# Performance work log

Measured on AMD Instinct MI355X. Metric: run time of the kernel, lower is better.

## Reference

```python
import jax, jax.numpy as jnp
import numpy as np

EPS = 1e-8

def quaternion_normalize(q):
    # q: [..., 4] -> unit quaternion
    return q / (jnp.linalg.norm(q, axis=-1, keepdims=True) + EPS)

def quaternion_mul(q1, q2):
    # Hamilton product; q1, q2 broadcastable [..., 4]
    w1, x1, y1, z1 = q1[..., 0], q1[..., 1], q1[..., 2], q1[..., 3]
    w2, x2, y2, z2 = q2[..., 0], q2[..., 1], q2[..., 2], q2[..., 3]
    w = w1 * w2 - x1 * x2 - y1 * y2 - z1 * z2
    x = w1 * x2 + x1 * w2 + y1 * z2 - z1 * y2
    y = w1 * y2 - x1 * z2 + y1 * w2 + z1 * x2
    z = w1 * z2 + x1 * y2 - y1 * x2 + z1 * w2
    return jnp.stack([w, x, y, z], axis=-1)

def setup_inputs() -> dict:
    key = jax.random.key(0)
    ks = jax.random.split(key, 7)
    B, N, M, D = 2, 512, 512, 256
    return {
        "vision_feat": jax.random.normal(ks[0], (B, N, D), dtype=jnp.float32),
        "text_feat": jax.random.normal(ks[1], (B, M, D), dtype=jnp.float32),
        "Wv": jax.random.normal(ks[2], (D, D), dtype=jnp.float32) * (1.0 / np.sqrt(D)),
        "bv": jax.random.normal(ks[3], (D,), dtype=jnp.float32) * 0.01,
        "Wt": jax.random.normal(ks[4], (D, D), dtype=jnp.float32) * (1.0 / np.sqrt(D)),
        "bt": jax.random.normal(ks[5], (D,), dtype=jnp.float32) * 0.01,
        "h": jnp.float32(1.0),
    }

def reference(vision_feat, text_feat, Wv, bv, Wt, bt, h):
    B, N, D = vision_feat.shape
    M = text_feat.shape[1]
    heads = D // 4
    # project to spinors and normalize per-quaternion
    v_spinor = quaternion_normalize((vision_feat @ Wv.T + bv).reshape(B, N, heads, 4))
    t_spinor = quaternion_normalize((text_feat @ Wt.T + bt).reshape(B, M, heads, 4))
    # broadcast pairwise quaternion product v * conj(t): [B, N, M, heads, 4]
    v_exp = v_spinor[:, :, None]                      # [B, N, 1, heads, 4]
    t_conj = t_spinor[:, None, :] * jnp.array([1.0, -1.0, -1.0, -1.0], dtype=t_spinor.dtype)
    inner = quaternion_mul(v_exp, t_conj)             # [B, N, M, heads, 4]
    vec_norm = jnp.linalg.norm(inner[..., 1:], axis=-1)
    w = inner[..., 0]
    gamma = 2.0 * jnp.arctan2(vec_norm, w + EPS)
    interference = jnp.cos(gamma / 2.0) ** 2          # [B, N, M, heads]
    attn = jax.nn.softmax(interference.mean(axis=-1) / jnp.sqrt(jnp.float32(D)), axis=-1)  # [B, N, M]
    new_vision = jnp.matmul(attn, text_feat)                      # [B, N, D]
    new_text = jnp.matmul(attn.transpose(0, 2, 1), vision_feat)   # [B, M, D]
    out_vision = vision_feat + h * new_vision
    out_text = text_feat + h * new_text
    return (out_vision, out_text)
```

## Files before the change

### kernel.cpp

```cpp
#include <hip/hip_runtime.h>
#include <math.h>

#define EPS 1e-8f

typedef short bf16x8 __attribute__((ext_vector_type(8)));
typedef short bf16x4 __attribute__((ext_vector_type(4)));
typedef float f32x4  __attribute__((ext_vector_type(4)));

__device__ __forceinline__ short f2bf(float f) {
    union { float fv; unsigned u; } v; v.fv = f;
    unsigned r = v.u + 0x7fffu + ((v.u >> 16) & 1u);
    return (short)(r >> 16);
}
__device__ __forceinline__ float bf2f(short s) {
    union { unsigned u; float f; } v;
    v.u = ((unsigned)(unsigned short)s) << 16;
    return v.f;
}
__device__ __forceinline__ bf16x8 pack8(float4 a, float4 b) {
    bf16x8 p;
    p[0] = f2bf(a.x); p[1] = f2bf(a.y); p[2] = f2bf(a.z); p[3] = f2bf(a.w);
    p[4] = f2bf(b.x); p[5] = f2bf(b.y); p[6] = f2bf(b.z); p[7] = f2bf(b.w);
    return p;
}

__global__ __launch_bounds__(256) void proj_expand_kernel(
    const float* __restrict__ vis, const float* __restrict__ txt,
    const float* __restrict__ Wv, const float* __restrict__ bv,
    const float* __restrict__ Wt, const float* __restrict__ bt,
    short* __restrict__ expq)
{
    const int t = threadIdx.x, lane = t & 63, wave = t >> 6;
    const int w  = blockIdx.x * 4 + wave;
    const int rt = w >> 3;
    const int ct = w & 7;
    const int which = rt >> 6;
    const int r0 = (rt & 63) * 16;
    const int c0 = ct * 32;
    const float* X    = which ? txt : vis;
    const float* W    = which ? Wt : Wv;
    const float* bias = which ? bt : bv;
    short* Eo = expq + which * 1024 * 1024;

    const int mrow = lane & 15, quad = lane >> 4;

    const float* Arow  = X + (r0 + mrow) * 256 + 8 * quad;
    const float* Brow0 = W + (c0 + mrow) * 256 + 8 * quad;
    const float* Brow1 = W + (c0 + 16 + mrow) * 256 + 8 * quad;

    f32x4 acc[2] = {};
    #pragma unroll 4
    for (int k0 = 0; k0 < 256; k0 += 32) {
        float4 a0 = *(const float4*)(Arow + k0);
        float4 a1 = *(const float4*)(Arow + k0 + 4);
        float4 p0 = *(const float4*)(Brow0 + k0);
        float4 p1 = *(const float4*)(Brow0 + k0 + 4);
        float4 q0 = *(const float4*)(Brow1 + k0);
        float4 q1 = *(const float4*)(Brow1 + k0 + 4);
        bf16x8 af = pack8(a0, a1);
        bf16x8 b0 = pack8(p0, p1);
        bf16x8 b1 = pack8(q0, q1);
        acc[0] = __builtin_amdgcn_mfma_f32_16x16x32_bf16(af, b0, acc[0], 0, 0, 0);
        acc[1] = __builtin_amdgcn_mfma_f32_16x16x32_bf16(af, b1, acc[1], 0, 0, 0);
    }

    const int qbase = lane & ~3;
    #pragma unroll
    for (int j = 0; j < 2; ++j) {
        const int col  = c0 + 16 * j + mrow;
        const float bb = bias[col];
        const int head = col >> 2;
        #pragma unroll
        for (int reg = 0; reg < 4; ++reg) {
            const int row = r0 + quad * 4 + reg;
            float v = acc[j][reg] + bb;
            float s = v * v;
            s += __shfl_xor(s, 1, 64);
            s += __shfl_xor(s, 2, 64);
            float q = v * (1.f / (sqrtf(s) + EPS));
            float q0 = __shfl(q, qbase + 0, 64);
            float q1 = __shfl(q, qbase + 1, 64);
            float q2 = __shfl(q, qbase + 2, 64);
            float q3 = __shfl(q, qbase + 3, 64);
            bf16x4 p;
            p[0] = f2bf(q * q0); p[1] = f2bf(q * q1);
            p[2] = f2bf(q * q2); p[3] = f2bf(q * q3);
            *(bf16x4*)(Eo + row * 1024 + head * 16 + (col & 3) * 4) = p;
        }
    }
}

__global__ __launch_bounds__(256) void logits_kernel(
    const short* __restrict__ expq, short* __restrict__ E,
    short* __restrict__ ET, float* __restrict__ rs)
{
    const int t = threadIdx.x, lane = t & 63, wave = t >> 6;
    const int w  = blockIdx.x * 4 + wave;
    const int b  = w >> 9;
    const int nt = (w >> 4) & 31;
    const int mt = w & 15;
    const int r0 = nt * 16, c0 = mt * 32;
    const int mrow = lane & 15, quad = lane >> 4;

    const short* Ar  = expq + (b * 512 + r0 + mrow) * 1024 + 8 * quad;
    const short* Br0 = expq + (1024 + b * 512 + c0 + mrow) * 1024 + 8 * quad;
    const short* Br1 = Br0 + 16 * 1024;

    f32x4 acc[2] = {};
    #pragma unroll 4
    for (int k0 = 0; k0 < 1024; k0 += 32) {
        bf16x8 a  = *(const bf16x8*)(Ar  + k0);
        bf16x8 b0 = *(const bf16x8*)(Br0 + k0);
        bf16x8 b1 = *(const bf16x8*)(Br1 + k0);
        acc[0] = __builtin_amdgcn_mfma_f32_16x16x32_bf16(a, b0, acc[0], 0, 0, 0);
        acc[1] = __builtin_amdgcn_mfma_f32_16x16x32_bf16(a, b1, acc[1], 0, 0, 0);
    }

    float e[2][4];
    #pragma unroll
    for (int j = 0; j < 2; ++j)
        #pragma unroll
        for (int reg = 0; reg < 4; ++reg)
            e[j][reg] = __expf(acc[j][reg] * (1.f / 1024.f));

    #pragma unroll
    for (int j = 0; j < 2; ++j) {
        const int col = c0 + 16 * j + mrow;
        bf16x4 pe;
        #pragma unroll
        for (int reg = 0; reg < 4; ++reg) {
            pe[reg] = f2bf(e[j][reg]);
            const int row = r0 + quad * 4 + reg;
            E[(b * 512 + row) * 512 + col] = pe[reg];
        }
        *(bf16x4*)(ET + (b * 512 + col) * 512 + r0 + quad * 4) = pe;
    }
    #pragma unroll
    for (int reg = 0; reg < 4; ++reg) {
        float p = e[0][reg] + e[1][reg];
        p += __shfl_xor(p, 1, 64);
        p += __shfl_xor(p, 2, 64);
        p += __shfl_xor(p, 4, 64);
        p += __shfl_xor(p, 8, 64);
        if (mrow == 0) {
            const int row = r0 + quad * 4 + reg;
            rs[(b * 512 + row) * 16 + (c0 >> 5)] = p;
        }
    }
}

__global__ __launch_bounds__(256) void transpose_scale_kernel(
    const float* __restrict__ vis, const float* __restrict__ txt,
    const float* __restrict__ rs,
    short* __restrict__ txtT, short* __restrict__ visST,
    float* __restrict__ rinv)
{
    const int bx = blockIdx.x;
    const int mat = bx >> 6;
    const int b   = (bx >> 5) & 1;
    const int m0  = (bx & 31) * 16;
    const int t   = threadIdx.x;

    __shared__ float rsc[16];
    if (mat == 1) {
        if (t < 16) {
            const float* p = rs + (b * 512 + m0 + t) * 16;
            float s = 0.f;
            #pragma unroll
            for (int i = 0; i < 16; ++i) s += p[i];
            const float ri = 1.f / s;
            rsc[t] = ri;
            rinv[b * 512 + m0 + t] = ri;
        }
        __syncthreads();
    }

    const float* src = (mat ? vis : txt) + (b * 512 + m0) * 256 + t;
    short* dst = (mat ? visST : txtT) + (b * 256 + t) * 512 + m0;

    bf16x8 v0, v1;
    #pragma unroll
    for (int i = 0; i < 8; ++i) {
        float a = src[i * 256];
        float c = src[(i + 8) * 256];
        if (mat) { a *= rsc[i]; c *= rsc[i + 8]; }
        v0[i] = f2bf(a);
        v1[i] = f2bf(c);
    }
    *(bf16x8*)(dst)     = v0;
    *(bf16x8*)(dst + 8) = v1;
}

__global__ __launch_bounds__(256) void out_kernel(
    const float* __restrict__ vis, const float* __restrict__ txt,
    const short* __restrict__ E, const short* __restrict__ ET,
    const short* __restrict__ txtT, const short* __restrict__ visST,
    const float* __restrict__ rinv, const float* __restrict__ hptr,
    float* __restrict__ outv, float* __restrict__ outt)
{
    const int t = threadIdx.x, lane = t & 63, wave = t >> 6;
    const int w     = blockIdx.x * 4 + wave;
    const int which = w >> 9;
    const int b     = (w >> 8) & 1;
    const int nt    = (w >> 3) & 31;
    const int dt    = w & 7;
    const int r0 = nt * 16, c0 = dt * 32;
    const int mrow = lane & 15, quad = lane >> 4;
    const float hv = hptr[0];

    const short* Ar  = (which ? ET : E) + (b * 512 + r0 + mrow) * 512 + 8 * quad;
    const short* Br0 = (which ? visST : txtT) + (b * 256 + c0 + mrow) * 512 + 8 * quad;
    const short* Br1 = Br0 + 16 * 512;
    const float* base = (which ? txt : vis) + (b * 512 + r0) * 256;
    float*       out  = (which ? outt : outv) + (b * 512 + r0) * 256;

    f32x4 acc[2] = {};
    #pragma unroll 4
    for (int k0 = 0; k0 < 512; k0 += 32) {
        bf16x8 a  = *(const bf16x8*)(Ar  + k0);
        bf16x8 b0 = *(const bf16x8*)(Br0 + k0);
        bf16x8 b1 = *(const bf16x8*)(Br1 + k0);
        acc[0] = __builtin_amdgcn_mfma_f32_16x16x32_bf16(a, b0, acc[0], 0, 0, 0);
        acc[1] = __builtin_amdgcn_mfma_f32_16x16x32_bf16(a, b1, acc[1], 0, 0, 0);
    }

    #pragma unroll
    for (int reg = 0; reg < 4; ++reg) {
        const int row = quad * 4 + reg;
        const float scale = which ? hv : hv * rinv[b * 512 + r0 + row];
        #pragma unroll
        for (int j = 0; j < 2; ++j) {
            const int col = c0 + 16 * j + mrow;
            out[row * 256 + col] = fmaf(scale, acc[j][reg], base[row * 256 + col]);
        }
    }
}

extern "C" void kernel_launch(void* const* d_in, const int* in_sizes, int n_in,
                              void* d_out, int out_size, void* d_ws, size_t ws_size,
                              hipStream_t stream)
{
    const float* vis = (const float*)d_in[0];
    const float* txt = (const float*)d_in[1];
    const float* Wv  = (const float*)d_in[2];
    const float* bv  = (const float*)d_in[3];
    const float* Wt  = (const float*)d_in[4];
    const float* bt  = (const float*)d_in[5];
    const float* h   = (const float*)d_in[6];

    float* outv = (float*)d_out;
    float* outt = (float*)d_out + 2 * 512 * 256;

    short* expq  = (short*)d_ws;
    short* E     = expq + 2048 * 1024;
    short* ET    = E + 1024 * 512;
    float* rs    = (float*)(ET + 1024 * 512);
    float* rinv  = rs + 1024 * 16;
    short* txtT  = (short*)(rinv + 1024);
    short* visST = txtT + 2 * 256 * 512;

    proj_expand_kernel<<<dim3(256), 256, 0, stream>>>(vis, txt, Wv, bv, Wt, bt, expq);
    logits_kernel<<<dim3(256), 256, 0, stream>>>(expq, E, ET, rs);
    transpose_scale_kernel<<<dim3(128), 256, 0, stream>>>(vis, txt, rs, txtT, visST, rinv);
    out_kernel<<<dim3(256), 256, 0, stream>>>(vis, txt, E, ET, txtT, visST, rinv, h, outv, outt);
}
```

Baseline: 103.7 us.

## Fuse four kernels into one cooperative kernel with grid-wide syncs

Replaces the four separate launches (projection/expand, logits, transpose/scale, output GEMM) with a single cooperative kernel of 512 blocks that separates the phases with grid.sync(). Each wave's tile is also halved to one 16x16 MFMA output so that 2048 waves cover every phase, and the row-sum partial buffer grows to 32 entries per row. This is meant to remove launch gaps and tail effects between stages. It costs grid-sync overhead, less per-wave data reuse (no shared A operand across two B tiles), and a cooperative-launch residency requirement.

```diff
diff --git a/kernel.cpp b/kernel.cpp
--- a/kernel.cpp
+++ b/kernel.cpp
@@ -1,5 +1,8 @@
 #include <hip/hip_runtime.h>
+#include <hip/hip_cooperative_groups.h>
 #include <math.h>
+
+namespace cg = cooperative_groups;
 
 #define EPS 1e-8f
 
@@ -11,11 +14,6 @@
     union { float fv; unsigned u; } v; v.fv = f;
     unsigned r = v.u + 0x7fffu + ((v.u >> 16) & 1u);
     return (short)(r >> 16);
-}
-__device__ __forceinline__ float bf2f(short s) {
-    union { unsigned u; float f; } v;
-    v.u = ((unsigned)(unsigned short)s) << 16;
-    return v.f;
 }
 __device__ __forceinline__ bf16x8 pack8(float4 a, float4 b) {
     bf16x8 p;
@@ -24,56 +22,54 @@
     return p;
 }
 
-__global__ __launch_bounds__(256) void proj_expand_kernel(
+__global__ __launch_bounds__(256, 2) void mega_kernel(
     const float* __restrict__ vis, const float* __restrict__ txt,
     const float* __restrict__ Wv, const float* __restrict__ bv,
     const float* __restrict__ Wt, const float* __restrict__ bt,
-    short* __restrict__ expq)
+    const float* __restrict__ hptr,
+    short* __restrict__ expq, short* __restrict__ E, short* __restrict__ ET,
+    float* __restrict__ rs, float* __restrict__ rinv,
+    short* __restrict__ txtT, short* __restrict__ visST,
+    float* __restrict__ outv, float* __restrict__ outt)
 {
+    cg::grid_group grid = cg::this_grid();
     const int t = threadIdx.x, lane = t & 63, wave = t >> 6;
-    const int w  = blockIdx.x * 4 + wave;
-    const int rt = w >> 3;
-    const int ct = w & 7;
-    const int which = rt >> 6;
-    const int r0 = (rt & 63) * 16;
-    const int c0 = ct * 32;
-    const float* X    = which ? txt : vis;
-    const float* W    = which ? Wt : Wv;
-    const float* bias = which ? bt : bv;
-    short* Eo = expq + which * 1024 * 1024;
-
+    const int w = blockIdx.x * 4 + wave;
     const int mrow = lane & 15, quad = lane >> 4;
 
-    const float* Arow  = X + (r0 + mrow) * 256 + 8 * quad;
-    const float* Brow0 = W + (c0 + mrow) * 256 + 8 * quad;
-    const float* Brow1 = W + (c0 + 16 + mrow) * 256 + 8 * quad;
-
-    f32x4 acc[2] = {};
-    #pragma unroll 4
-    for (int k0 = 0; k0 < 256; k0 += 32) {
-        float4 a0 = *(const float4*)(Arow + k0);
-        float4 a1 = *(const float4*)(Arow + k0 + 4);
-        float4 p0 = *(const float4*)(Brow0 + k0);
-        float4 p1 = *(const float4*)(Brow0 + k0 + 4);
-        float4 q0 = *(const float4*)(Brow1 + k0);
-        float4 q1 = *(const float4*)(Brow1 + k0 + 4);
-        bf16x8 af = pack8(a0, a1);
-        bf16x8 b0 = pack8(p0, p1);
-        bf16x8 b1 = pack8(q0, q1);
-        acc[0] = __builtin_amdgcn_mfma_f32_16x16x32_bf16(af, b0, acc[0], 0, 0, 0);
-        acc[1] = __builtin_amdgcn_mfma_f32_16x16x32_bf16(af, b1, acc[1], 0, 0, 0);
-    }
-
-    const int qbase = lane & ~3;
-    #pragma unroll
-    for (int j = 0; j < 2; ++j) {
-        const int col  = c0 + 16 * j + mrow;
+    {
+        const int rt = w >> 4;
+        const int ct = w & 15;
+        const int which = rt >> 6;
+        const int r0 = (rt & 63) * 16, c0 = ct * 16;
+        const float* X    = which ? txt : vis;
+        const float* W    = which ? Wt : Wv;
+        const float* bias = which ? bt : bv;
+        short* Eo = expq + which * 1024 * 1024;
+
+        const float* Arow = X + (r0 + mrow) * 256 + 8 * quad;
+        const float* Brow = W + (c0 + mrow) * 256 + 8 * quad;
+
+        f32x4 acc = {};
+        #pragma unroll 2
+        for (int k0 = 0; k0 < 256; k0 += 32) {
+            float4 a0 = *(const float4*)(Arow + k0);
+            float4 a1 = *(const float4*)(Arow + k0 + 4);
+            float4 b0 = *(const float4*)(Brow + k0);
+            float4 b1 = *(const float4*)(Brow + k0 + 4);
+            bf16x8 af = pack8(a0, a1);
+            bf16x8 bf = pack8(b0, b1);
+            acc = __builtin_amdgcn_mfma_f32_16x16x32_bf16(af, bf, acc, 0, 0, 0);
+        }
+
+        const int col  = c0 + mrow;
         const float bb = bias[col];
         const int head = col >> 2;
+        const int qbase = lane & ~3;
         #pragma unroll
         for (int reg = 0; reg < 4; ++reg) {
             const int row = r0 + quad * 4 + reg;
-            float v = acc[j][reg] + bb;
+            float v = acc[reg] + bb;
             float s = v * v;
             s += __shfl_xor(s, 1, 64);
             s += __shfl_xor(s, 2, 64);
@@ -88,150 +84,114 @@
             *(bf16x4*)(Eo + row * 1024 + head * 16 + (col & 3) * 4) = p;
         }
     }
-}
-
-__global__ __launch_bounds__(256) void logits_kernel(
-    const short* __restrict__ expq, short* __restrict__ E,
-    short* __restrict__ ET, float* __restrict__ rs)
-{
-    const int t = threadIdx.x, lane = t & 63, wave = t >> 6;
-    const int w  = blockIdx.x * 4 + wave;
-    const int b  = w >> 9;
-    const int nt = (w >> 4) & 31;
-    const int mt = w & 15;
-    const int r0 = nt * 16, c0 = mt * 32;
-    const int mrow = lane & 15, quad = lane >> 4;
-
-    const short* Ar  = expq + (b * 512 + r0 + mrow) * 1024 + 8 * quad;
-    const short* Br0 = expq + (1024 + b * 512 + c0 + mrow) * 1024 + 8 * quad;
-    const short* Br1 = Br0 + 16 * 1024;
-
-    f32x4 acc[2] = {};
-    #pragma unroll 4
-    for (int k0 = 0; k0 < 1024; k0 += 32) {
-        bf16x8 a  = *(const bf16x8*)(Ar  + k0);
-        bf16x8 b0 = *(const bf16x8*)(Br0 + k0);
-        bf16x8 b1 = *(const bf16x8*)(Br1 + k0);
-        acc[0] = __builtin_amdgcn_mfma_f32_16x16x32_bf16(a, b0, acc[0], 0, 0, 0);
-        acc[1] = __builtin_amdgcn_mfma_f32_16x16x32_bf16(a, b1, acc[1], 0, 0, 0);
-    }
-
-    float e[2][4];
-    #pragma unroll
-    for (int j = 0; j < 2; ++j)
-        #pragma unroll
-        for (int reg = 0; reg < 4; ++reg)
-            e[j][reg] = __expf(acc[j][reg] * (1.f / 1024.f));
-
-    #pragma unroll
-    for (int j = 0; j < 2; ++j) {
-        const int col = c0 + 16 * j + mrow;
+    grid.sync();
+
+    {
+        const int b  = w >> 10;
+        const int nt = (w >> 5) & 31;
+        const int mt = w & 31;
+        const int r0 = nt * 16, c0 = mt * 16;
+
+        const short* Ar = expq + (b * 512 + r0 + mrow) * 1024 + 8 * quad;
+        const short* Br = expq + (1024 + b * 512 + c0 + mrow) * 1024 + 8 * quad;
+
+        f32x4 acc = {};
+        #pragma unroll 8
+        for (int k0 = 0; k0 < 1024; k0 += 32) {
+            bf16x8 a  = *(const bf16x8*)(Ar + k0);
+            bf16x8 bf = *(const bf16x8*)(Br + k0);
+            acc = __builtin_amdgcn_mfma_f32_16x16x32_bf16(a, bf, acc, 0, 0, 0);
+        }
+
+        float e[4];
         bf16x4 pe;
-        #pragma unroll
-        for (int reg = 0; reg < 4; ++reg) {
-            pe[reg] = f2bf(e[j][reg]);
+        const int col = c0 + mrow;
+        #pragma unroll
+        for (int reg = 0; reg < 4; ++reg) {
+            e[reg] = __expf(acc[reg] * (1.f / 1024.f));
+            pe[reg] = f2bf(e[reg]);
             const int row = r0 + quad * 4 + reg;
             E[(b * 512 + row) * 512 + col] = pe[reg];
         }
         *(bf16x4*)(ET + (b * 512 + col) * 512 + r0 + quad * 4) = pe;
-    }
-    #pragma unroll
-    for (int reg = 0; reg < 4; ++reg) {
-        float p = e[0][reg] + e[1][reg];
-        p += __shfl_xor(p, 1, 64);
-        p += __shfl_xor(p, 2, 64);
-        p += __shfl_xor(p, 4, 64);
-        p += __shfl_xor(p, 8, 64);
-        if (mrow == 0) {
-            const int row = r0 + quad * 4 + reg;
-            rs[(b * 512 + row) * 16 + (c0 >> 5)] = p;
-        }
-    }
-}
-
-__global__ __launch_bounds__(256) void transpose_scale_kernel(
-    const float* __restrict__ vis, const float* __restrict__ txt,
-    const float* __restrict__ rs,
-    short* __restrict__ txtT, short* __restrict__ visST,
-    float* __restrict__ rinv)
-{
-    const int bx = blockIdx.x;
-    const int mat = bx >> 6;
-    const int b   = (bx >> 5) & 1;
-    const int m0  = (bx & 31) * 16;
-    const int t   = threadIdx.x;
-
-    __shared__ float rsc[16];
-    if (mat == 1) {
-        if (t < 16) {
-            const float* p = rs + (b * 512 + m0 + t) * 16;
-            float s = 0.f;
+        #pragma unroll
+        for (int reg = 0; reg < 4; ++reg) {
+            float p = e[reg];
+            p += __shfl_xor(p, 1, 64);
+            p += __shfl_xor(p, 2, 64);
+            p += __shfl_xor(p, 4, 64);
+            p += __shfl_xor(p, 8, 64);
+            if (mrow == 0) {
+                const int row = r0 + quad * 4 + reg;
+                rs[(b * 512 + row) * 32 + mt] = p;
+            }
+        }
+    }
+    grid.sync();
+
+    {
+        const int bx = blockIdx.x;
+        if (bx < 256) {
+            const int mat = bx >> 7;
+            const int b   = (bx >> 6) & 1;
+            const int m0  = (bx & 63) * 8;
+
+            __shared__ float rsc[8];
+            if (mat == 1) {
+                if (t < 8) {
+                    const float* p = rs + (b * 512 + m0 + t) * 32;
+                    float s = 0.f;
+                    #pragma unroll
+                    for (int i = 0; i < 32; ++i) s += p[i];
+                    const float ri = 1.f / s;
+                    rsc[t] = ri;
+                    rinv[b * 512 + m0 + t] = ri;
+                }
+                __syncthreads();
+            }
+
+            const float* src = (mat ? vis : txt) + (b * 512 + m0) * 256 + t;
+            short* dst = (mat ? visST : txtT) + (b * 256 + t) * 512 + m0;
+
+            bf16x8 v0;
             #pragma unroll
-            for (int i = 0; i < 16; ++i) s += p[i];
-            const float ri = 1.f / s;
-            rsc[t] = ri;
-            rinv[b * 512 + m0 + t] = ri;
-        }
-        __syncthreads();
-    }
-
-    const float* src = (mat ? vis : txt) + (b * 512 + m0) * 256 + t;
-    short* dst = (mat ? visST : txtT) + (b * 256 + t) * 512 + m0;
-
-    bf16x8 v0, v1;
-    #pragma unroll
-    for (int i = 0; i < 8; ++i) {
-        float a = src[i * 256];
-        float c = src[(i + 8) * 256];
-        if (mat) { a *= rsc[i]; c *= rsc[i + 8]; }
-        v0[i] = f2bf(a);
-        v1[i] = f2bf(c);
-    }
-    *(bf16x8*)(dst)     = v0;
-    *(bf16x8*)(dst + 8) = v1;
-}
-
-__global__ __launch_bounds__(256) void out_kernel(
-    const float* __restrict__ vis, const float* __restrict__ txt,
-    const short* __restrict__ E, const short* __restrict__ ET,
-    const short* __restrict__ txtT, const short* __restrict__ visST,
-    const float* __restrict__ rinv, const float* __restrict__ hptr,
-    float* __restrict__ outv, float* __restrict__ outt)
-{
-    const int t = threadIdx.x, lane = t & 63, wave = t >> 6;
-    const int w     = blockIdx.x * 4 + wave;
-    const int which = w >> 9;
-    const int b     = (w >> 8) & 1;
-    const int nt    = (w >> 3) & 31;
-    const int dt    = w & 7;
-    const int r0 = nt * 16, c0 = dt * 32;
-    const int mrow = lane & 15, quad = lane >> 4;
-    const float hv = hptr[0];
-
-    const short* Ar  = (which ? ET : E) + (b * 512 + r0 + mrow) * 512 + 8 * quad;
-    const short* Br0 = (which ? visST : txtT) + (b * 256 + c0 + mrow) * 512 + 8 * quad;
-    const short* Br1 = Br0 + 16 * 512;
-    const float* base = (which ? txt : vis) + (b * 512 + r0) * 256;
-    float*       out  = (which ? outt : outv) + (b * 512 + r0) * 256;
-
-    f32x4 acc[2] = {};
-    #pragma unroll 4
-    for (int k0 = 0; k0 < 512; k0 += 32) {
-        bf16x8 a  = *(const bf16x8*)(Ar  + k0);
-        bf16x8 b0 = *(const bf16x8*)(Br0 + k0);
-        bf16x8 b1 = *(const bf16x8*)(Br1 + k0);
-        acc[0] = __builtin_amdgcn_mfma_f32_16x16x32_bf16(a, b0, acc[0], 0, 0, 0);
-        acc[1] = __builtin_amdgcn_mfma_f32_16x16x32_bf16(a, b1, acc[1], 0, 0, 0);
-    }
-
-    #pragma unroll
-    for (int reg = 0; reg < 4; ++reg) {
-        const int row = quad * 4 + reg;
-        const float scale = which ? hv : hv * rinv[b * 512 + r0 + row];
-        #pragma unroll
-        for (int j = 0; j < 2; ++j) {
-            const int col = c0 + 16 * j + mrow;
-            out[row * 256 + col] = fmaf(scale, acc[j][reg], base[row * 256 + col]);
+            for (int i = 0; i < 8; ++i) {
+                float a = src[i * 256];
+                if (mat) a *= rsc[i];
+                v0[i] = f2bf(a);
+            }
+            *(bf16x8*)dst = v0;
+        }
+    }
+    grid.sync();
+
+    {
+        const int which = w >> 10;
+        const int b     = (w >> 9) & 1;
+        const int nt    = (w >> 4) & 31;
+        const int dt    = w & 15;
+        const int r0 = nt * 16, c0 = dt * 16;
+        const float hv = hptr[0];
+
+        const short* Ar = (which ? ET : E) + (b * 512 + r0 + mrow) * 512 + 8 * quad;
+        const short* Br = (which ? visST : txtT) + (b * 256 + c0 + mrow) * 512 + 8 * quad;
+        const float* base = (which ? txt : vis) + (b * 512 + r0) * 256;
+        float*       out  = (which ? outt : outv) + (b * 512 + r0) * 256;
+
+        f32x4 acc = {};
+        #pragma unroll 8
+        for (int k0 = 0; k0 < 512; k0 += 32) {
+            bf16x8 a  = *(const bf16x8*)(Ar + k0);
+            bf16x8 bf = *(const bf16x8*)(Br + k0);
+            acc = __builtin_amdgcn_mfma_f32_16x16x32_bf16(a, bf, acc, 0, 0, 0);
+        }
+
+        const int col = c0 + mrow;
+        #pragma unroll
+        for (int reg = 0; reg < 4; ++reg) {
+            const int row = quad * 4 + reg;
+            const float scale = which ? hv : hv * rinv[b * 512 + r0 + row];
+            out[row * 256 + col] = fmaf(scale, acc[reg], base[row * 256 + col]);
         }
     }
 }
@@ -255,12 +215,14 @@
     short* E     = expq + 2048 * 1024;
     short* ET    = E + 1024 * 512;
     float* rs    = (float*)(ET + 1024 * 512);
-    float* rinv  = rs + 1024 * 16;
+    float* rinv  = rs + 1024 * 32;
     short* txtT  = (short*)(rinv + 1024);
     short* visST = txtT + 2 * 256 * 512;
 
-    proj_expand_kernel<<<dim3(256), 256, 0, stream>>>(vis, txt, Wv, bv, Wt, bt, expq);
-    logits_kernel<<<dim3(256), 256, 0, stream>>>(expq, E, ET, rs);
-    transpose_scale_kernel<<<dim3(128), 256, 0, stream>>>(vis, txt, rs, txtT, visST, rinv);
-    out_kernel<<<dim3(256), 256, 0, stream>>>(vis, txt, E, ET, txtT, visST, rinv, h, outv, outt);
-}
+    void* args[] = {
+        (void*)&vis, (void*)&txt, (void*)&Wv, (void*)&bv, (void*)&Wt, (void*)&bt,
+        (void*)&h, (void*)&expq, (void*)&E, (void*)&ET, (void*)&rs, (void*)&rinv,
+        (void*)&txtT, (void*)&visST, (void*)&outv, (void*)&outt
+    };
+    hipLaunchCooperativeKernel(mega_kernel, dim3(512), dim3(256), args, 0, stream);
+}
```

New measurement: 278.9 us. +169.0%, slower.
